# Kernel tuning notes

Measured on AMD Instinct MI355X. Metric: run time of the kernel, lower is better.

The kernel has to match this reference:

```python
import jax, jax.numpy as jnp
import numpy as np

NUM_HEADS = 8
GROUPS = 8
EPS = 1e-5


def setup_inputs() -> dict:
    key = jax.random.key(0)
    ks = jax.random.split(key, 5)
    B, C, H, W = 2, 512, 64, 64
    x = jax.random.normal(ks[0], (B, C, H, W), dtype=jnp.float32)
    gn_w = jnp.ones((C,), dtype=jnp.float32)
    gn_b = jnp.zeros((C,), dtype=jnp.float32)
    qkv_w = jax.random.normal(ks[1], (3 * C, C), dtype=jnp.float32) * 0.02  # 1x1 conv weight
    qkv_b = jnp.zeros((3 * C,), dtype=jnp.float32)
    proj_w = jax.random.normal(ks[2], (C, C), dtype=jnp.float32) * 0.02
    proj_b = jnp.zeros((C,), dtype=jnp.float32)
    return {"x": x, "gn_w": gn_w, "gn_b": gn_b, "qkv_w": qkv_w,
            "qkv_b": qkv_b, "proj_w": proj_w, "proj_b": proj_b}


def group_norm(x, w, b):
    B, C, H, W = x.shape
    xg = x.reshape(B, GROUPS, C // GROUPS, H, W)
    mean = xg.mean(axis=(2, 3, 4), keepdims=True)
    var = xg.var(axis=(2, 3, 4), keepdims=True)  # biased, matching torch GroupNorm
    h = ((xg - mean) * jax.lax.rsqrt(var + EPS)).reshape(B, C, H, W)
    return h * w[None, :, None, None] + b[None, :, None, None]


def reference(x, gn_w, gn_b, qkv_w, qkv_b, proj_w, proj_b):
    B, C, H, W = x.shape
    nh = NUM_HEADS
    dh = C // nh
    scale = dh ** -0.5
    S = H * W

    h = group_norm(x, gn_w, gn_b)
    # 1x1 conv == per-pixel linear: (B,3C,H,W)
    qkv = jnp.einsum('bchw,oc->bohw', h, qkv_w) + qkv_b[None, :, None, None]
    qkv = qkv.reshape(B, 3, nh, dh, S)
    q = jnp.swapaxes(qkv[:, 0], -1, -2)  # (B, nh, S, dh)
    k = jnp.swapaxes(qkv[:, 1], -1, -2)
    v = jnp.swapaxes(qkv[:, 2], -1, -2)

    attn = jax.nn.softmax(jnp.einsum('bhsd,btd->bhst', q, k.reshape(B * nh, S, dh).reshape(B, nh, S, dh)) * scale, axis=-1) if False else jax.nn.softmax(jnp.einsum('bhsd,bhtd->bhst', q, k) * scale, axis=-1)
    out = jnp.einsum('bhst,bhtd->bhsd', attn, v)  # (B, nh, S, dh)
    out = jnp.swapaxes(out, -1, -2).reshape(B, C, H, W)
    out = jnp.einsum('bchw,oc->bohw', out, proj_w) + proj_b[None, :, None, None]
    return x + out
```

## Files before the change

kernel.cpp:

```cpp
#include <hip/hip_runtime.h>
#include <hip/hip_bf16.h>

typedef __attribute__((ext_vector_type(4)))  float  f32x4;
typedef __attribute__((ext_vector_type(16))) float  f32x16;
typedef __attribute__((ext_vector_type(8)))  short  s16x8;
typedef __attribute__((ext_vector_type(4)))  short  s16x4;
typedef __attribute__((ext_vector_type(4)))  unsigned u32x4;
typedef __attribute__((ext_vector_type(2)))  unsigned u32x2;

__device__ __forceinline__ float bf2f(short v) {
    unsigned u = ((unsigned)(unsigned short)v) << 16;
    return __builtin_bit_cast(float, u);
}
__device__ __forceinline__ short f2bf(float f) {
    unsigned u = __builtin_bit_cast(unsigned, f);
    u += 0x7fff + ((u >> 16) & 1);
    return (short)(u >> 16);
}
__device__ __forceinline__ unsigned cvt_pk_bf16(float lo, float hi) {
    unsigned r;
    asm("v_cvt_pk_bf16_f32 %0, %1, %2" : "=v"(r) : "v"(lo), "v"(hi));
    return r;
}
__device__ __forceinline__ float exp2_asm(float x) {
    float r; asm("v_exp_f32 %0, %1" : "=v"(r) : "v"(x)); return r;
}
__device__ __forceinline__ float log2_asm(float x) {
    float r; asm("v_log_f32 %0, %1" : "=v"(r) : "v"(x)); return r;
}
__device__ __forceinline__ void perm32swap(unsigned &a, unsigned &b) {
    u32x2 r = __builtin_amdgcn_permlane32_swap(a, b, false, false);
    a = r[0]; b = r[1];
}
__device__ __forceinline__ void gload16(const short* g, short* l) {
    __builtin_amdgcn_global_load_lds(
        (const __attribute__((address_space(1))) void*)g,
        (__attribute__((address_space(3))) void*)l, 16, 0, 0);
}

#define BATCH 2
#define CCH   512
#define SSP   4096
#define NH    8
#define DH    64

__global__ __launch_bounds__(256) void gn_partial_wcast_kernel(
    const float* __restrict__ x, float* __restrict__ part,
    const float* __restrict__ qw, const float* __restrict__ pw,
    short* __restrict__ dq, short* __restrict__ dp)
{
    if (blockIdx.x >= 512) {
        int idx = ((blockIdx.x - 512) * 256 + threadIdx.x) * 8;
        const float* src; short* dst;
        if (idx < 786432) { src = qw + idx; dst = dq + idx; }
        else              { src = pw + (idx - 786432); dst = dp + (idx - 786432); }
        f32x4 a = *(const f32x4*)src;
        f32x4 b = *(const f32x4*)(src + 4);
        s16x8 o;
        o[0]=f2bf(a[0]); o[1]=f2bf(a[1]); o[2]=f2bf(a[2]); o[3]=f2bf(a[3]);
        o[4]=f2bf(b[0]); o[5]=f2bf(b[1]); o[6]=f2bf(b[2]); o[7]=f2bf(b[3]);
        *(s16x8*)dst = o;
        return;
    }
    int bg = blockIdx.x >> 5, chunk = blockIdx.x & 31;
    const float* base = x + (size_t)bg * 262144 + chunk * 8192;
    int t = threadIdx.x, lane = t & 63, wave = t >> 6;
    float s = 0.f, ss = 0.f;
    #pragma unroll
    for (int k = 0; k < 8; ++k) {
        f32x4 v = *(const f32x4*)&base[k * 1024 + t * 4];
        #pragma unroll
        for (int j = 0; j < 4; ++j) { s += v[j]; ss += v[j] * v[j]; }
    }
    #pragma unroll
    for (int mask = 1; mask < 64; mask <<= 1) {
        s  += __shfl_xor(s,  mask);
        ss += __shfl_xor(ss, mask);
    }
    __shared__ float rs[4], rss[4];
    if (lane == 0) { rs[wave] = s; rss[wave] = ss; }
    __syncthreads();
    if (t == 0) {
        part[blockIdx.x * 2]     = rs[0] + rs[1] + rs[2] + rs[3];
        part[blockIdx.x * 2 + 1] = rss[0] + rss[1] + rss[2] + rss[3];
    }
}

__global__ void gn_final_kernel(const float* __restrict__ part, float* __restrict__ stats)
{
    int t = threadIdx.x;
    if (t < 16) {
        float s = 0.f, ss = 0.f;
        for (int c = 0; c < 32; ++c) {
            s  += part[(t * 32 + c) * 2];
            ss += part[(t * 32 + c) * 2 + 1];
        }
        float mean = s * (1.f / 262144.f);
        float var  = ss * (1.f / 262144.f) - mean * mean;
        stats[t * 2]     = mean;
        stats[t * 2 + 1] = rsqrtf(var + 1e-5f);
    }
}

__global__ __launch_bounds__(256) void gn_apply_kernel(
    const float* __restrict__ x, const float* __restrict__ gw, const float* __restrict__ gb,
    const float* __restrict__ stats, short* __restrict__ hbuf)
{
    __shared__ float tile[64][65];
    int id = blockIdx.x;
    int st = id & 63, ct = (id >> 6) & 7, b = id >> 9;
    int t  = threadIdx.x;
    float mean = stats[(b * 8 + ct) * 2], rstd = stats[(b * 8 + ct) * 2 + 1];
    #pragma unroll
    for (int pass = 0; pass < 4; ++pass) {
        int cr = pass * 16 + (t >> 4);
        int c  = ct * 64 + cr;
        f32x4 v = *(const f32x4*)&x[((size_t)(b * CCH + c)) * SSP + st * 64 + (t & 15) * 4];
        float w  = gw[c] * rstd;
        float bb = gb[c] - mean * w;
        #pragma unroll
        for (int j = 0; j < 4; ++j) tile[cr][(t & 15) * 4 + j] = v[j] * w + bb;
    }
    __syncthreads();
    int sr = t >> 2, cc0 = (t & 3) * 16;
    s16x8 o0, o1;
    #pragma unroll
    for (int j = 0; j < 8; ++j) {
        o0[j] = f2bf(tile[cc0 + j][sr]);
        o1[j] = f2bf(tile[cc0 + 8 + j][sr]);
    }
    short* dst = &hbuf[(size_t)(b * SSP + st * 64 + sr) * CCH + ct * 64 + cc0];
    *(s16x8*)dst = o0;
    *(s16x8*)(dst + 8) = o1;
}

template<int EPI>
__global__ __launch_bounds__(256) void gemm_bt_kernel(
    const short* __restrict__ A, const short* __restrict__ Bt,
    const float* __restrict__ bias,
    short* __restrict__ qout, short* __restrict__ kout, short* __restrict__ vout,
    const float* __restrict__ xres, float* __restrict__ out,
    int K)
{
    __shared__ short As[4096], Bs[4096];
    const int t = threadIdx.x;
    const int lane = t & 63, wave = t >> 6;
    const int wm = wave >> 1, wn = wave & 1;
    const int flat = blockIdx.y * 64 + blockIdx.x;
    const int m0 = (((flat & 7) << 3) + ((flat >> 3) & 7)) * 128;
    const int n0 = (flat >> 6) * 128;
    const int l15 = lane & 15, lq = lane >> 4;

    f32x4 acc[4][4];
    #pragma unroll
    for (int i = 0; i < 4; ++i)
        #pragma unroll
        for (int j = 0; j < 4; ++j) acc[i][j] = (f32x4){0.f, 0.f, 0.f, 0.f};

    for (int kk = 0; kk < K; kk += 32) {
        __syncthreads();
        #pragma unroll
        for (int i = 0; i < 2; ++i) {
            int idx = i * 256 + t;
            int row = idx >> 2, cb = idx & 3;
            int dst = ((row >> 4) << 9) + ((((row & 15)) | (cb << 4)) << 3);
            *(s16x8*)&As[dst] = *(const s16x8*)&A [(size_t)(m0 + row) * K + kk + cb * 8];
            *(s16x8*)&Bs[dst] = *(const s16x8*)&Bt[(size_t)(n0 + row) * K + kk + cb * 8];
        }
        __syncthreads();
        s16x8 af[4], bfr[4];
        #pragma unroll
        for (int mt = 0; mt < 4; ++mt) af[mt]  = *(const s16x8*)&As[(((wm * 4 + mt) << 9) + lane * 8)];
        #pragma unroll
        for (int nt = 0; nt < 4; ++nt) bfr[nt] = *(const s16x8*)&Bs[(((wn * 4 + nt) << 9) + lane * 8)];
        #pragma unroll
        for (int mt = 0; mt < 4; ++mt)
            #pragma unroll
            for (int nt = 0; nt < 4; ++nt)
                acc[mt][nt] = __builtin_amdgcn_mfma_f32_16x16x32_bf16(af[mt], bfr[nt], acc[mt][nt], 0, 0, 0);
    }

    #pragma unroll
    for (int mt = 0; mt < 4; ++mt) {
        const int r0 = m0 + wm * 64 + mt * 16 + lq * 4;
        #pragma unroll
        for (int nt = 0; nt < 4; ++nt) {
            const int c = n0 + wn * 64 + nt * 16 + l15;
            float bv = bias[c];
            if (EPI == 0) {
                int bb = r0 >> 12, tloc = r0 & 4095;
                if (c < 512) {
                    #pragma unroll
                    for (int i = 0; i < 4; ++i)
                        qout[(size_t)(r0 + i) * 512 + c] = f2bf(acc[mt][nt][i] + bv);
                } else if (c < 1024) {
                    int hh = (c - 512) >> 6, d = (c - 512) & 63;
                    int T = tloc >> 6, tb = (tloc >> 5) & 1;
                    size_t base = (((size_t)(bb * 8 + hh) * 64 + T) * 8 + tb * 4 + (d >> 4)) * 512
                                  + 256 * ((d >> 3) & 1) + (d & 7);
                    #pragma unroll
                    for (int i = 0; i < 4; ++i)
                        kout[base + ((tloc & 31) + i) * 8] = f2bf(acc[mt][nt][i] + bv);
                } else {
                    int hh = (c - 1024) >> 6, d = (c - 1024) & 63;
                    int T = tloc >> 6, s = (tloc >> 4) & 3, thi = (tloc >> 3) & 1, j0 = tloc & 7;
                    size_t base = (((size_t)(bb * 8 + hh) * 64 + T) * 8 + (d >> 5) * 4 + s) * 512
                                  + ((d & 31) + 32 * thi) * 8 + j0;
                    s16x4 pv;
                    #pragma unroll
                    for (int i = 0; i < 4; ++i) pv[i] = f2bf(acc[mt][nt][i] + bv);
                    *(s16x4*)&vout[base] = pv;
                }
            } else {
                int bb = r0 >> 12, s = r0 & 4095;
                size_t xi = (size_t)(bb * CCH + c) * SSP + s;
                f32x4 xv = *(const f32x4*)&xres[xi];
                f32x4 o  = xv + acc[mt][nt] + bv;
                *(f32x4*)&out[xi] = o;
            }
        }
    }
}

__global__ __launch_bounds__(256, 4) void attn_kernel(
    const short* __restrict__ qbuf, const short* __restrict__ kfrag,
    const short* __restrict__ vfrag,
    short* __restrict__ p0, short* __restrict__ p1, float* __restrict__ aout)
{
    __shared__ short Ks[2][4096];
    __shared__ short Vs[2][4096];
    const int t = threadIdx.x, lane = t & 63, wave = t >> 6;
    const int flat = blockIdx.y * 32 + blockIdx.x;
    const int p = flat >> 3;
    const int yy = (flat & 7) * 4 + (p & 3);
    const int qblk = p >> 2;
    const int bh = yy & 15, half = yy >> 4;
    const int b = bh >> 3, h = bh & 7;
    const int q0w = qblk * 128 + wave * 32;
    const int l31 = lane & 31, lh = lane >> 5;
    const int kv0 = half * 2048;

    s16x8 qf[4];
    {
        const short* qp = qbuf + (size_t)(b * SSP + q0w + l31) * 512 + h * 64 + 8 * lh;
        #pragma unroll
        for (int s = 0; s < 4; ++s) {
            s16x8 raw = *(const s16x8*)(qp + 16 * s);
            #pragma unroll
            for (int j = 0; j < 8; ++j) qf[s][j] = f2bf(bf2f(raw[j]) * 0.18033688011112042f);
        }
    }

    const short* kbase = kfrag + (size_t)bh * 262144 + lane * 8;
    const short* vbase = vfrag + (size_t)bh * 262144 + lane * 8;

    f32x16 oacc[2];
    oacc[0] = (f32x16){}; oacc[1] = (f32x16){};
    f32x16 lacc = (f32x16){};

    s16x8 ones;
    #pragma unroll
    for (int j = 0; j < 8; ++j) ones[j] = (short)0x3F80;

    {
        const short* kg = kbase + (size_t)(kv0 >> 6) * 4096 + wave * 1024;
        gload16(kg,       &Ks[0][wave * 1024]);
        gload16(kg + 512, &Ks[0][wave * 1024 + 512]);
        const short* vg = vbase + (size_t)(kv0 >> 6) * 4096 + wave * 1024;
        gload16(vg,       &Vs[0][wave * 1024]);
        gload16(vg + 512, &Vs[0][wave * 1024 + 512]);
    }
    asm volatile("s_waitcnt vmcnt(0)" ::: "memory");
    __syncthreads();

    int cur = 0;
    for (int t0 = kv0; t0 < kv0 + 2048; t0 += 64) {
        if (t0 + 64 < kv0 + 2048) {
            int nb = cur ^ 1;
            const short* kg = kbase + (size_t)((t0 + 64) >> 6) * 4096 + wave * 1024;
            gload16(kg,       &Ks[nb][wave * 1024]);
            gload16(kg + 512, &Ks[nb][wave * 1024 + 512]);
            const short* vg = vbase + (size_t)((t0 + 64) >> 6) * 4096 + wave * 1024;
            gload16(vg,       &Vs[nb][wave * 1024]);
            gload16(vg + 512, &Vs[nb][wave * 1024 + 512]);
        }

        f32x16 sacc0 = (f32x16){}, sacc1 = (f32x16){};
        __builtin_amdgcn_s_setprio(1);
        #pragma unroll
        for (int s = 0; s < 4; ++s) {
            s16x8 k0 = *(const s16x8*)&Ks[cur][(0 + s) * 512 + lane * 8];
            s16x8 k1 = *(const s16x8*)&Ks[cur][(4 + s) * 512 + lane * 8];
            sacc0 = __builtin_amdgcn_mfma_f32_32x32x16_bf16(k0, qf[s], sacc0, 0, 0, 0);
            sacc1 = __builtin_amdgcn_mfma_f32_32x32x16_bf16(k1, qf[s], sacc1, 0, 0, 0);
        }
        __builtin_amdgcn_s_setprio(0);

        #pragma unroll
        for (int r = 0; r < 16; ++r) { sacc0[r] = exp2_asm(sacc0[r]); sacc1[r] = exp2_asm(sacc1[r]); }

        unsigned w[16];
        #pragma unroll
        for (int r = 0; r < 8; ++r) {
            w[r]     = cvt_pk_bf16(sacc0[2 * r], sacc0[2 * r + 1]);
            w[8 + r] = cvt_pk_bf16(sacc1[2 * r], sacc1[2 * r + 1]);
        }
        #pragma unroll
        for (int s = 0; s < 4; ++s) {
            perm32swap(w[s * 4 + 0], w[s * 4 + 2]);
            perm32swap(w[s * 4 + 1], w[s * 4 + 3]);
        }

        __builtin_amdgcn_s_setprio(1);
        #pragma unroll
        for (int s = 0; s < 4; ++s) {
            u32x4 pb = { w[s * 4 + 0], w[s * 4 + 1], w[s * 4 + 2], w[s * 4 + 3] };
            s16x8 pB = __builtin_bit_cast(s16x8, pb);
            s16x8 v0v = *(const s16x8*)&Vs[cur][(0 + s) * 512 + lane * 8];
            s16x8 v1v = *(const s16x8*)&Vs[cur][(4 + s) * 512 + lane * 8];
            oacc[0] = __builtin_amdgcn_mfma_f32_32x32x16_bf16(v0v, pB, oacc[0], 0, 0, 0);
            oacc[1] = __builtin_amdgcn_mfma_f32_32x32x16_bf16(v1v, pB, oacc[1], 0, 0, 0);
            lacc    = __builtin_amdgcn_mfma_f32_32x32x16_bf16(ones, pB, lacc, 0, 0, 0);
        }
        __builtin_amdgcn_s_setprio(0);

        asm volatile("s_waitcnt vmcnt(0)" ::: "memory");
        __syncthreads();
        cur ^= 1;
    }

    short* pO = half ? p1 : p0;
    float l_ = lacc[0];
    float linv = 1.f / l_;
    int q = q0w + l31;
    size_t obase = ((size_t)bh * 4096 + q) * 64;
    #pragma unroll
    for (int db = 0; db < 2; ++db)
        #pragma unroll
        for (int g = 0; g < 4; ++g) {
            s16x4 o;
            #pragma unroll
            for (int i = 0; i < 4; ++i) o[i] = f2bf(oacc[db][g * 4 + i] * linv);
            *(s16x4*)&pO[obase + db * 32 + g * 8 + lh * 4] = o;
        }
    if (lh == 0)
        aout[half * 65536 + bh * 4096 + q] = log2_asm(l_);
}

__global__ __launch_bounds__(256) void combine_kernel(
    const short* __restrict__ p0, const short* __restrict__ p1,
    const float* __restrict__ aout, short* __restrict__ ao)
{
    int bh = blockIdx.x >> 7, q = (blockIdx.x & 127) * 32 + (threadIdx.x >> 3);
    int d0 = (threadIdx.x & 7) * 8;
    size_t pi = ((size_t)bh * 4096 + q) * 64 + d0;
    s16x8 o1 = *(const s16x8*)&p0[pi];
    s16x8 o2 = *(const s16x8*)&p1[pi];
    float a1 = aout[bh * 4096 + q], a2 = aout[65536 + bh * 4096 + q];
    float M = fmaxf(a1, a2);
    float w1 = exp2_asm(a1 - M), w2 = exp2_asm(a2 - M);
    float inv = 1.f / (w1 + w2);
    w1 *= inv; w2 *= inv;
    s16x8 o;
    #pragma unroll
    for (int j = 0; j < 8; ++j) o[j] = f2bf(bf2f(o1[j]) * w1 + bf2f(o2[j]) * w2);
    int b = bh >> 3, h = bh & 7;
    *(s16x8*)&ao[(size_t)(b * SSP + q) * 512 + h * 64 + d0] = o;
}

extern "C" void kernel_launch(void* const* d_in, const int* in_sizes, int n_in,
                              void* d_out, int out_size, void* d_ws, size_t ws_size,
                              hipStream_t stream)
{
    (void)in_sizes; (void)n_in; (void)out_size; (void)ws_size;
    const float* x      = (const float*)d_in[0];
    const float* gn_w   = (const float*)d_in[1];
    const float* gn_b   = (const float*)d_in[2];
    const float* qkv_w  = (const float*)d_in[3];
    const float* qkv_b  = (const float*)d_in[4];
    const float* proj_w = (const float*)d_in[5];
    const float* proj_b = (const float*)d_in[6];
    float* out = (float*)d_out;
    char* ws = (char*)d_ws;

    short* hbuf  = (short*)(ws + 0);
    short* qbuf  = (short*)(ws + 8388608);
    short* kfrag = (short*)(ws + 16777216);
    short* vfrag = (short*)(ws + 25165824);
    short* aobuf = (short*)(ws + 33554432);
    short* wqkv  = (short*)(ws + 41943040);
    short* wproj = (short*)(ws + 43515904);
    float* part  = (float*)(ws + 44040192);
    float* stats = (float*)(ws + 44044288);
    float* ascal = (float*)(ws + 41943040);

    gn_partial_wcast_kernel<<<1024, 256, 0, stream>>>(x, part, qkv_w, proj_w, wqkv, wproj);
    gn_final_kernel<<<1, 64, 0, stream>>>(part, stats);
    gn_apply_kernel<<<1024, 256, 0, stream>>>(x, gn_w, gn_b, stats, hbuf);
    gemm_bt_kernel<0><<<dim3(64, 12), 256, 0, stream>>>(hbuf, wqkv, qkv_b,
                                                        qbuf, kfrag, vfrag, nullptr, nullptr, 512);
    attn_kernel<<<dim3(32, 32), 256, 0, stream>>>(qbuf, kfrag, vfrag,
                                                  hbuf, aobuf, ascal);
    combine_kernel<<<2048, 256, 0, stream>>>(hbuf, aobuf, ascal, kfrag);
    gemm_bt_kernel<1><<<dim3(64, 4), 256, 0, stream>>>(kfrag, wproj, proj_b,
                                                       nullptr, nullptr, nullptr, x, out, 512);
}
```

Measured before the change: 149.1 us.

## Software-pipeline attention: overlap QK of next tile with PV of previous, scalar row-sum

Restructures the attention inner loop so that the QK^T MFMAs for tile T are issued together with the PV MFMAs for tile T-1. This lets the exp2 and bf16 packing of one tile overlap with matrix work, and it needs a third V shared-memory buffer plus ping-pong P registers. The row-sum is also no longer computed by an extra MFMA against a ones vector. Instead it is accumulated with scalar adds over the exp values and combined across half-waves with a shuffle. The cost is higher register pressure from carrying the P fragments across iterations, plus more LDS use, which could reduce occupancy.

```diff
diff --git a/kernel.cpp b/kernel.cpp
--- a/kernel.cpp
+++ b/kernel.cpp
@@ -228,7 +228,7 @@
     short* __restrict__ p0, short* __restrict__ p1, float* __restrict__ aout)
 {
     __shared__ short Ks[2][4096];
-    __shared__ short Vs[2][4096];
+    __shared__ short Vs[3][4096];
     const int t = threadIdx.x, lane = t & 63, wave = t >> 6;
     const int flat = blockIdx.y * 32 + blockIdx.x;
     const int p = flat >> 3;
@@ -238,7 +238,7 @@
     const int b = bh >> 3, h = bh & 7;
     const int q0w = qblk * 128 + wave * 32;
     const int l31 = lane & 31, lh = lane >> 5;
-    const int kv0 = half * 2048;
+    const int tile0 = half * 32;
 
     s16x8 qf[4];
     {
@@ -256,81 +256,100 @@
 
     f32x16 oacc[2];
     oacc[0] = (f32x16){}; oacc[1] = (f32x16){};
-    f32x16 lacc = (f32x16){};
-
-    s16x8 ones;
-    #pragma unroll
-    for (int j = 0; j < 8; ++j) ones[j] = (short)0x3F80;
+    float l_ = 0.f;
+    s16x8 pA[4], pB[4];
+
+    int kcur = 0, knext = 1, vprev = 2, vcur = 0, vnext = 1;
 
     {
-        const short* kg = kbase + (size_t)(kv0 >> 6) * 4096 + wave * 1024;
+        const short* kg = kbase + (size_t)tile0 * 4096 + wave * 1024;
         gload16(kg,       &Ks[0][wave * 1024]);
         gload16(kg + 512, &Ks[0][wave * 1024 + 512]);
-        const short* vg = vbase + (size_t)(kv0 >> 6) * 4096 + wave * 1024;
+        const short* vg = vbase + (size_t)tile0 * 4096 + wave * 1024;
         gload16(vg,       &Vs[0][wave * 1024]);
         gload16(vg + 512, &Vs[0][wave * 1024 + 512]);
     }
     asm volatile("s_waitcnt vmcnt(0)" ::: "memory");
     __syncthreads();
 
-    int cur = 0;
-    for (int t0 = kv0; t0 < kv0 + 2048; t0 += 64) {
-        if (t0 + 64 < kv0 + 2048) {
-            int nb = cur ^ 1;
-            const short* kg = kbase + (size_t)((t0 + 64) >> 6) * 4096 + wave * 1024;
-            gload16(kg,       &Ks[nb][wave * 1024]);
-            gload16(kg + 512, &Ks[nb][wave * 1024 + 512]);
-            const short* vg = vbase + (size_t)((t0 + 64) >> 6) * 4096 + wave * 1024;
-            gload16(vg,       &Vs[nb][wave * 1024]);
-            gload16(vg + 512, &Vs[nb][wave * 1024 + 512]);
-        }
-
-        f32x16 sacc0 = (f32x16){}, sacc1 = (f32x16){};
-        __builtin_amdgcn_s_setprio(1);
-        #pragma unroll
-        for (int s = 0; s < 4; ++s) {
-            s16x8 k0 = *(const s16x8*)&Ks[cur][(0 + s) * 512 + lane * 8];
-            s16x8 k1 = *(const s16x8*)&Ks[cur][(4 + s) * 512 + lane * 8];
-            sacc0 = __builtin_amdgcn_mfma_f32_32x32x16_bf16(k0, qf[s], sacc0, 0, 0, 0);
-            sacc1 = __builtin_amdgcn_mfma_f32_32x32x16_bf16(k1, qf[s], sacc1, 0, 0, 0);
-        }
-        __builtin_amdgcn_s_setprio(0);
-
-        #pragma unroll
-        for (int r = 0; r < 16; ++r) { sacc0[r] = exp2_asm(sacc0[r]); sacc1[r] = exp2_asm(sacc1[r]); }
-
-        unsigned w[16];
-        #pragma unroll
-        for (int r = 0; r < 8; ++r) {
-            w[r]     = cvt_pk_bf16(sacc0[2 * r], sacc0[2 * r + 1]);
-            w[8 + r] = cvt_pk_bf16(sacc1[2 * r], sacc1[2 * r + 1]);
-        }
-        #pragma unroll
-        for (int s = 0; s < 4; ++s) {
-            perm32swap(w[s * 4 + 0], w[s * 4 + 2]);
-            perm32swap(w[s * 4 + 1], w[s * 4 + 3]);
-        }
-
-        __builtin_amdgcn_s_setprio(1);
-        #pragma unroll
-        for (int s = 0; s < 4; ++s) {
-            u32x4 pb = { w[s * 4 + 0], w[s * 4 + 1], w[s * 4 + 2], w[s * 4 + 3] };
-            s16x8 pB = __builtin_bit_cast(s16x8, pb);
-            s16x8 v0v = *(const s16x8*)&Vs[cur][(0 + s) * 512 + lane * 8];
-            s16x8 v1v = *(const s16x8*)&Vs[cur][(4 + s) * 512 + lane * 8];
-            oacc[0] = __builtin_amdgcn_mfma_f32_32x32x16_bf16(v0v, pB, oacc[0], 0, 0, 0);
-            oacc[1] = __builtin_amdgcn_mfma_f32_32x32x16_bf16(v1v, pB, oacc[1], 0, 0, 0);
-            lacc    = __builtin_amdgcn_mfma_f32_32x32x16_bf16(ones, pB, lacc, 0, 0, 0);
-        }
-        __builtin_amdgcn_s_setprio(0);
-
-        asm volatile("s_waitcnt vmcnt(0)" ::: "memory");
-        __syncthreads();
-        cur ^= 1;
-    }
-
+#define ATTN_STEP(T, PIN, POUT, HAS_NEXT, DO_PV)                                  \
+    {                                                                             \
+        if (HAS_NEXT) {                                                           \
+            const short* kg = kbase + (size_t)(tile0 + (T) + 1) * 4096 + wave * 1024; \
+            gload16(kg,       &Ks[knext][wave * 1024]);                           \
+            gload16(kg + 512, &Ks[knext][wave * 1024 + 512]);                     \
+            const short* vg = vbase + (size_t)(tile0 + (T) + 1) * 4096 + wave * 1024; \
+            gload16(vg,       &Vs[vnext][wave * 1024]);                           \
+            gload16(vg + 512, &Vs[vnext][wave * 1024 + 512]);                     \
+        }                                                                         \
+        f32x16 sacc0 = (f32x16){}, sacc1 = (f32x16){};                            \
+        __builtin_amdgcn_s_setprio(1);                                            \
+        _Pragma("unroll")                                                         \
+        for (int s = 0; s < 4; ++s) {                                             \
+            s16x8 k0 = *(const s16x8*)&Ks[kcur][(0 + s) * 512 + lane * 8];        \
+            s16x8 k1 = *(const s16x8*)&Ks[kcur][(4 + s) * 512 + lane * 8];        \
+            sacc0 = __builtin_amdgcn_mfma_f32_32x32x16_bf16(k0, qf[s], sacc0, 0, 0, 0); \
+            sacc1 = __builtin_amdgcn_mfma_f32_32x32x16_bf16(k1, qf[s], sacc1, 0, 0, 0); \
+        }                                                                         \
+        if (DO_PV) {                                                              \
+            _Pragma("unroll")                                                     \
+            for (int s = 0; s < 4; ++s) {                                         \
+                s16x8 v0v = *(const s16x8*)&Vs[vprev][(0 + s) * 512 + lane * 8];  \
+                s16x8 v1v = *(const s16x8*)&Vs[vprev][(4 + s) * 512 + lane * 8];  \
+                oacc[0] = __builtin_amdgcn_mfma_f32_32x32x16_bf16(v0v, PIN[s], oacc[0], 0, 0, 0); \
+                oacc[1] = __builtin_amdgcn_mfma_f32_32x32x16_bf16(v1v, PIN[s], oacc[1], 0, 0, 0); \
+            }                                                                     \
+        }                                                                         \
+        __builtin_amdgcn_s_setprio(0);                                            \
+        float a0 = 0.f, a1 = 0.f, a2 = 0.f, a3 = 0.f;                             \
+        _Pragma("unroll")                                                         \
+        for (int r = 0; r < 8; ++r) {                                             \
+            sacc0[r]     = exp2_asm(sacc0[r]);     a0 += sacc0[r];                \
+            sacc0[8 + r] = exp2_asm(sacc0[8 + r]); a1 += sacc0[8 + r];            \
+            sacc1[r]     = exp2_asm(sacc1[r]);     a2 += sacc1[r];                \
+            sacc1[8 + r] = exp2_asm(sacc1[8 + r]); a3 += sacc1[8 + r];            \
+        }                                                                         \
+        l_ += (a0 + a1) + (a2 + a3);                                              \
+        unsigned w_[16];                                                          \
+        _Pragma("unroll")                                                         \
+        for (int r = 0; r < 8; ++r) {                                             \
+            w_[r]     = cvt_pk_bf16(sacc0[2 * r], sacc0[2 * r + 1]);              \
+            w_[8 + r] = cvt_pk_bf16(sacc1[2 * r], sacc1[2 * r + 1]);              \
+        }                                                                         \
+        _Pragma("unroll")                                                         \
+        for (int s = 0; s < 4; ++s) {                                             \
+            perm32swap(w_[s * 4 + 0], w_[s * 4 + 2]);                             \
+            perm32swap(w_[s * 4 + 1], w_[s * 4 + 3]);                             \
+            u32x4 pb4 = { w_[s * 4 + 0], w_[s * 4 + 1], w_[s * 4 + 2], w_[s * 4 + 3] }; \
+            POUT[s] = __builtin_bit_cast(s16x8, pb4);                             \
+        }                                                                         \
+        asm volatile("s_waitcnt vmcnt(0)" ::: "memory");                          \
+        __syncthreads();                                                          \
+        kcur ^= 1; knext ^= 1;                                                    \
+        int vtmp = vprev; vprev = vcur; vcur = vnext; vnext = vtmp;               \
+    }
+
+    ATTN_STEP(0, pA, pA, true, false)
+    for (int tp = 0; tp < 15; ++tp) {
+        int t1 = 2 * tp + 1;
+        ATTN_STEP(t1,     pA, pB, true, true)
+        ATTN_STEP(t1 + 1, pB, pA, true, true)
+    }
+    ATTN_STEP(31, pA, pB, false, true)
+#undef ATTN_STEP
+
+    __builtin_amdgcn_s_setprio(1);
+    #pragma unroll
+    for (int s = 0; s < 4; ++s) {
+        s16x8 v0v = *(const s16x8*)&Vs[vprev][(0 + s) * 512 + lane * 8];
+        s16x8 v1v = *(const s16x8*)&Vs[vprev][(4 + s) * 512 + lane * 8];
+        oacc[0] = __builtin_amdgcn_mfma_f32_32x32x16_bf16(v0v, pB[s], oacc[0], 0, 0, 0);
+        oacc[1] = __builtin_amdgcn_mfma_f32_32x32x16_bf16(v1v, pB[s], oacc[1], 0, 0, 0);
+    }
+    __builtin_amdgcn_s_setprio(0);
+
+    l_ += __shfl_xor(l_, 32);
     short* pO = half ? p1 : p0;
-    float l_ = lacc[0];
     float linv = 1.f / l_;
     int q = q0w + l31;
     size_t obase = ((size_t)bh * 4096 + q) * 64;
```

Result: no change. 146.4 us (-1.9%).

## Double query rows per wave in attention, fuse GN finalize into apply

Applied to the files above, without the earlier changes.

Each attention wave now handles 64 query rows instead of 32, so every K/V tile loaded into LDS feeds twice as many MFMAs and the grid is halved. The row-sum is accumulated with VALU adds instead of an extra MFMA against a ones vector, saving one matrix op per step. The separate GroupNorm finalize launch is removed; each apply block reduces the 32 partials itself with shuffles, and the apply kernel packs bf16 pairs before the LDS transpose to shrink the tile. Register pressure rises and occupancy drops to 2 blocks per CU, so latency hiding may suffer.

```diff
diff --git a/kernel.cpp b/kernel.cpp
--- a/kernel.cpp
+++ b/kernel.cpp
@@ -86,52 +86,55 @@
     }
 }
 
-__global__ void gn_final_kernel(const float* __restrict__ part, float* __restrict__ stats)
-{
-    int t = threadIdx.x;
-    if (t < 16) {
-        float s = 0.f, ss = 0.f;
-        for (int c = 0; c < 32; ++c) {
-            s  += part[(t * 32 + c) * 2];
-            ss += part[(t * 32 + c) * 2 + 1];
-        }
-        float mean = s * (1.f / 262144.f);
-        float var  = ss * (1.f / 262144.f) - mean * mean;
-        stats[t * 2]     = mean;
-        stats[t * 2 + 1] = rsqrtf(var + 1e-5f);
-    }
-}
-
 __global__ __launch_bounds__(256) void gn_apply_kernel(
     const float* __restrict__ x, const float* __restrict__ gw, const float* __restrict__ gb,
-    const float* __restrict__ stats, short* __restrict__ hbuf)
-{
-    __shared__ float tile[64][65];
+    const float* __restrict__ part, short* __restrict__ hbuf)
+{
+    __shared__ unsigned tile[32][66];
     int id = blockIdx.x;
     int st = id & 63, ct = (id >> 6) & 7, b = id >> 9;
     int t  = threadIdx.x;
-    float mean = stats[(b * 8 + ct) * 2], rstd = stats[(b * 8 + ct) * 2 + 1];
-    #pragma unroll
-    for (int pass = 0; pass < 4; ++pass) {
-        int cr = pass * 16 + (t >> 4);
-        int c  = ct * 64 + cr;
-        f32x4 v = *(const f32x4*)&x[((size_t)(b * CCH + c)) * SSP + st * 64 + (t & 15) * 4];
-        float w  = gw[c] * rstd;
-        float bb = gb[c] - mean * w;
-        #pragma unroll
-        for (int j = 0; j < 4; ++j) tile[cr][(t & 15) * 4 + j] = v[j] * w + bb;
+
+    int bg = b * 8 + ct;
+    float s  = part[(bg * 32 + (t & 31)) * 2];
+    float ss = part[(bg * 32 + (t & 31)) * 2 + 1];
+    #pragma unroll
+    for (int m = 1; m < 32; m <<= 1) { s += __shfl_xor(s, m); ss += __shfl_xor(ss, m); }
+    float mean = s * (1.f / 262144.f);
+    float var  = ss * (1.f / 262144.f) - mean * mean;
+    float rstd = rsqrtf(var + 1e-5f);
+
+    #pragma unroll
+    for (int pass = 0; pass < 2; ++pass) {
+        int cp = pass * 16 + (t >> 4);
+        int c  = ct * 64 + cp * 2;
+        const float* xp = &x[((size_t)(b * CCH + c)) * SSP + st * 64 + (t & 15) * 4];
+        f32x4 v0 = *(const f32x4*)xp;
+        f32x4 v1 = *(const f32x4*)(xp + SSP);
+        float w0 = gw[c] * rstd,     bb0 = gb[c] - mean * w0;
+        float w1 = gw[c + 1] * rstd, bb1 = gb[c + 1] - mean * w1;
+        int sp0 = (t & 15) * 4;
+        unsigned p0 = cvt_pk_bf16(v0[0] * w0 + bb0, v1[0] * w1 + bb1);
+        unsigned p1 = cvt_pk_bf16(v0[1] * w0 + bb0, v1[1] * w1 + bb1);
+        unsigned p2 = cvt_pk_bf16(v0[2] * w0 + bb0, v1[2] * w1 + bb1);
+        unsigned p3 = cvt_pk_bf16(v0[3] * w0 + bb0, v1[3] * w1 + bb1);
+        *(u32x2*)&tile[cp][sp0]     = (u32x2){p0, p1};
+        *(u32x2*)&tile[cp][sp0 + 2] = (u32x2){p2, p3};
     }
     __syncthreads();
-    int sr = t >> 2, cc0 = (t & 3) * 16;
-    s16x8 o0, o1;
-    #pragma unroll
-    for (int j = 0; j < 8; ++j) {
-        o0[j] = f2bf(tile[cc0 + j][sr]);
-        o1[j] = f2bf(tile[cc0 + 8 + j][sr]);
-    }
-    short* dst = &hbuf[(size_t)(b * SSP + st * 64 + sr) * CCH + ct * 64 + cc0];
-    *(s16x8*)dst = o0;
-    *(s16x8*)(dst + 8) = o1;
+
+    int sr = t >> 2, c16 = (t & 3) * 8;
+    unsigned r0 = tile[c16 + 0][sr];
+    unsigned r1 = tile[c16 + 1][sr];
+    unsigned r2 = tile[c16 + 2][sr];
+    unsigned r3 = tile[c16 + 3][sr];
+    unsigned r4 = tile[c16 + 4][sr];
+    unsigned r5 = tile[c16 + 5][sr];
+    unsigned r6 = tile[c16 + 6][sr];
+    unsigned r7 = tile[c16 + 7][sr];
+    short* dst = &hbuf[(size_t)(b * SSP + st * 64 + sr) * CCH + ct * 64 + c16 * 2];
+    *(u32x4*)dst       = (u32x4){r0, r1, r2, r3};
+    *(u32x4*)(dst + 8) = (u32x4){r4, r5, r6, r7};
 }
 
 template<int EPI>
@@ -222,7 +225,7 @@
     }
 }
 
-__global__ __launch_bounds__(256, 4) void attn_kernel(
+__global__ __launch_bounds__(256, 2) void attn_kernel(
     const short* __restrict__ qbuf, const short* __restrict__ kfrag,
     const short* __restrict__ vfrag,
     short* __restrict__ p0, short* __restrict__ p1, float* __restrict__ aout)
@@ -230,43 +233,43 @@
     __shared__ short Ks[2][4096];
     __shared__ short Vs[2][4096];
     const int t = threadIdx.x, lane = t & 63, wave = t >> 6;
-    const int flat = blockIdx.y * 32 + blockIdx.x;
+    const int flat = blockIdx.y * 16 + blockIdx.x;
     const int p = flat >> 3;
     const int yy = (flat & 7) * 4 + (p & 3);
     const int qblk = p >> 2;
     const int bh = yy & 15, half = yy >> 4;
     const int b = bh >> 3, h = bh & 7;
-    const int q0w = qblk * 128 + wave * 32;
+    const int q0w = qblk * 256 + wave * 64;
     const int l31 = lane & 31, lh = lane >> 5;
-    const int kv0 = half * 2048;
-
-    s16x8 qf[4];
+    const int tile0 = half * 32;
+
+    s16x8 qfa[4], qfb[4];
     {
-        const short* qp = qbuf + (size_t)(b * SSP + q0w + l31) * 512 + h * 64 + 8 * lh;
+        const short* qpa = qbuf + (size_t)(b * SSP + q0w + l31) * 512 + h * 64 + 8 * lh;
+        const short* qpb = qpa + 32 * 512;
         #pragma unroll
         for (int s = 0; s < 4; ++s) {
-            s16x8 raw = *(const s16x8*)(qp + 16 * s);
+            s16x8 ra = *(const s16x8*)(qpa + 16 * s);
+            s16x8 rb = *(const s16x8*)(qpb + 16 * s);
             #pragma unroll
-            for (int j = 0; j < 8; ++j) qf[s][j] = f2bf(bf2f(raw[j]) * 0.18033688011112042f);
+            for (int j = 0; j < 8; ++j) {
+                qfa[s][j] = f2bf(bf2f(ra[j]) * 0.18033688011112042f);
+                qfb[s][j] = f2bf(bf2f(rb[j]) * 0.18033688011112042f);
+            }
         }
     }
 
     const short* kbase = kfrag + (size_t)bh * 262144 + lane * 8;
     const short* vbase = vfrag + (size_t)bh * 262144 + lane * 8;
 
-    f32x16 oacc[2];
-    oacc[0] = (f32x16){}; oacc[1] = (f32x16){};
-    f32x16 lacc = (f32x16){};
-
-    s16x8 ones;
-    #pragma unroll
-    for (int j = 0; j < 8; ++j) ones[j] = (short)0x3F80;
+    f32x16 oa0 = (f32x16){}, oa1 = (f32x16){}, ob0 = (f32x16){}, ob1 = (f32x16){};
+    float la = 0.f, lb = 0.f;
 
     {
-        const short* kg = kbase + (size_t)(kv0 >> 6) * 4096 + wave * 1024;
+        const short* kg = kbase + (size_t)tile0 * 4096 + wave * 1024;
         gload16(kg,       &Ks[0][wave * 1024]);
         gload16(kg + 512, &Ks[0][wave * 1024 + 512]);
-        const short* vg = vbase + (size_t)(kv0 >> 6) * 4096 + wave * 1024;
+        const short* vg = vbase + (size_t)tile0 * 4096 + wave * 1024;
         gload16(vg,       &Vs[0][wave * 1024]);
         gload16(vg + 512, &Vs[0][wave * 1024 + 512]);
     }
@@ -274,53 +277,71 @@
     __syncthreads();
 
     int cur = 0;
-    for (int t0 = kv0; t0 < kv0 + 2048; t0 += 64) {
-        if (t0 + 64 < kv0 + 2048) {
+    for (int ti = 0; ti < 32; ++ti) {
+        if (ti + 1 < 32) {
             int nb = cur ^ 1;
-            const short* kg = kbase + (size_t)((t0 + 64) >> 6) * 4096 + wave * 1024;
+            const short* kg = kbase + (size_t)(tile0 + ti + 1) * 4096 + wave * 1024;
             gload16(kg,       &Ks[nb][wave * 1024]);
             gload16(kg + 512, &Ks[nb][wave * 1024 + 512]);
-            const short* vg = vbase + (size_t)((t0 + 64) >> 6) * 4096 + wave * 1024;
+            const short* vg = vbase + (size_t)(tile0 + ti + 1) * 4096 + wave * 1024;
             gload16(vg,       &Vs[nb][wave * 1024]);
             gload16(vg + 512, &Vs[nb][wave * 1024 + 512]);
         }
 
-        f32x16 sacc0 = (f32x16){}, sacc1 = (f32x16){};
+        f32x16 sa0 = (f32x16){}, sa1 = (f32x16){}, sb0 = (f32x16){}, sb1 = (f32x16){};
         __builtin_amdgcn_s_setprio(1);
         #pragma unroll
         for (int s = 0; s < 4; ++s) {
             s16x8 k0 = *(const s16x8*)&Ks[cur][(0 + s) * 512 + lane * 8];
             s16x8 k1 = *(const s16x8*)&Ks[cur][(4 + s) * 512 + lane * 8];
-            sacc0 = __builtin_amdgcn_mfma_f32_32x32x16_bf16(k0, qf[s], sacc0, 0, 0, 0);
-            sacc1 = __builtin_amdgcn_mfma_f32_32x32x16_bf16(k1, qf[s], sacc1, 0, 0, 0);
+            sa0 = __builtin_amdgcn_mfma_f32_32x32x16_bf16(k0, qfa[s], sa0, 0, 0, 0);
+            sa1 = __builtin_amdgcn_mfma_f32_32x32x16_bf16(k1, qfa[s], sa1, 0, 0, 0);
+            sb0 = __builtin_amdgcn_mfma_f32_32x32x16_bf16(k0, qfb[s], sb0, 0, 0, 0);
+            sb1 = __builtin_amdgcn_mfma_f32_32x32x16_bf16(k1, qfb[s], sb1, 0, 0, 0);
         }
         __builtin_amdgcn_s_setprio(0);
 
-        #pragma unroll
-        for (int r = 0; r < 16; ++r) { sacc0[r] = exp2_asm(sacc0[r]); sacc1[r] = exp2_asm(sacc1[r]); }
-
-        unsigned w[16];
+        float aa0 = 0.f, aa1 = 0.f, ab0 = 0.f, ab1 = 0.f;
+        #pragma unroll
+        for (int r = 0; r < 16; ++r) {
+            sa0[r] = exp2_asm(sa0[r]); aa0 += sa0[r];
+            sa1[r] = exp2_asm(sa1[r]); aa1 += sa1[r];
+            sb0[r] = exp2_asm(sb0[r]); ab0 += sb0[r];
+            sb1[r] = exp2_asm(sb1[r]); ab1 += sb1[r];
+        }
+        la += aa0 + aa1;
+        lb += ab0 + ab1;
+
+        unsigned wa[16], wb[16];
         #pragma unroll
         for (int r = 0; r < 8; ++r) {
-            w[r]     = cvt_pk_bf16(sacc0[2 * r], sacc0[2 * r + 1]);
-            w[8 + r] = cvt_pk_bf16(sacc1[2 * r], sacc1[2 * r + 1]);
-        }
+            wa[r]     = cvt_pk_bf16(sa0[2 * r], sa0[2 * r + 1]);
+            wa[8 + r] = cvt_pk_bf16(sa1[2 * r], sa1[2 * r + 1]);
+            wb[r]     = cvt_pk_bf16(sb0[2 * r], sb0[2 * r + 1]);
+            wb[8 + r] = cvt_pk_bf16(sb1[2 * r], sb1[2 * r + 1]);
+        }
+        s16x8 pa[4], pb[4];
         #pragma unroll
         for (int s = 0; s < 4; ++s) {
-            perm32swap(w[s * 4 + 0], w[s * 4 + 2]);
-            perm32swap(w[s * 4 + 1], w[s * 4 + 3]);
+            perm32swap(wa[s * 4 + 0], wa[s * 4 + 2]);
+            perm32swap(wa[s * 4 + 1], wa[s * 4 + 3]);
+            u32x4 pa4 = { wa[s * 4 + 0], wa[s * 4 + 1], wa[s * 4 + 2], wa[s * 4 + 3] };
+            pa[s] = __builtin_bit_cast(s16x8, pa4);
+            perm32swap(wb[s * 4 + 0], wb[s * 4 + 2]);
+            perm32swap(wb[s * 4 + 1], wb[s * 4 + 3]);
+            u32x4 pb4 = { wb[s * 4 + 0], wb[s * 4 + 1], wb[s * 4 + 2], wb[s * 4 + 3] };
+            pb[s] = __builtin_bit_cast(s16x8, pb4);
         }
 
         __builtin_amdgcn_s_setprio(1);
         #pragma unroll
         for (int s = 0; s < 4; ++s) {
-            u32x4 pb = { w[s * 4 + 0], w[s * 4 + 1], w[s * 4 + 2], w[s * 4 + 3] };
-            s16x8 pB = __builtin_bit_cast(s16x8, pb);
             s16x8 v0v = *(const s16x8*)&Vs[cur][(0 + s) * 512 + lane * 8];
             s16x8 v1v = *(const s16x8*)&Vs[cur][(4 + s) * 512 + lane * 8];
-            oacc[0] = __builtin_amdgcn_mfma_f32_32x32x16_bf16(v0v, pB, oacc[0], 0, 0, 0);
-            oacc[1] = __builtin_amdgcn_mfma_f32_32x32x16_bf16(v1v, pB, oacc[1], 0, 0, 0);
-            lacc    = __builtin_amdgcn_mfma_f32_32x32x16_bf16(ones, pB, lacc, 0, 0, 0);
+            oa0 = __builtin_amdgcn_mfma_f32_32x32x16_bf16(v0v, pa[s], oa0, 0, 0, 0);
+            oa1 = __builtin_amdgcn_mfma_f32_32x32x16_bf16(v1v, pa[s], oa1, 0, 0, 0);
+            ob0 = __builtin_amdgcn_mfma_f32_32x32x16_bf16(v0v, pb[s], ob0, 0, 0, 0);
+            ob1 = __builtin_amdgcn_mfma_f32_32x32x16_bf16(v1v, pb[s], ob1, 0, 0, 0);
         }
         __builtin_amdgcn_s_setprio(0);
 
@@ -330,21 +351,44 @@
     }
 
     short* pO = half ? p1 : p0;
-    float l_ = lacc[0];
-    float linv = 1.f / l_;
-    int q = q0w + l31;
-    size_t obase = ((size_t)bh * 4096 + q) * 64;
-    #pragma unroll
-    for (int db = 0; db < 2; ++db)
+    {
+        la += __shfl_xor(la, 32);
+        float linv = 1.f / la;
+        int q = q0w + l31;
+        size_t obase = ((size_t)bh * 4096 + q) * 64;
         #pragma unroll
         for (int g = 0; g < 4; ++g) {
-            s16x4 o;
+            s16x4 o0v, o1v;
             #pragma unroll
-            for (int i = 0; i < 4; ++i) o[i] = f2bf(oacc[db][g * 4 + i] * linv);
-            *(s16x4*)&pO[obase + db * 32 + g * 8 + lh * 4] = o;
-        }
-    if (lh == 0)
-        aout[half * 65536 + bh * 4096 + q] = log2_asm(l_);
+            for (int i = 0; i < 4; ++i) {
+                o0v[i] = f2bf(oa0[g * 4 + i] * linv);
+                o1v[i] = f2bf(oa1[g * 4 + i] * linv);
+            }
+            *(s16x4*)&pO[obase + g * 8 + lh * 4]      = o0v;
+            *(s16x4*)&pO[obase + 32 + g * 8 + lh * 4] = o1v;
+        }
+        if (lh == 0)
+            aout[half * 65536 + bh * 4096 + q] = log2_asm(la);
+    }
+    {
+        lb += __shfl_xor(lb, 32);
+        float linv = 1.f / lb;
+        int q = q0w + 32 + l31;
+        size_t obase = ((size_t)bh * 4096 + q) * 64;
+        #pragma unroll
+        for (int g = 0; g < 4; ++g) {
+            s16x4 o0v, o1v;
+            #pragma unroll
+            for (int i = 0; i < 4; ++i) {
+                o0v[i] = f2bf(ob0[g * 4 + i] * linv);
+                o1v[i] = f2bf(ob1[g * 4 + i] * linv);
+            }
+            *(s16x4*)&pO[obase + g * 8 + lh * 4]      = o0v;
+            *(s16x4*)&pO[obase + 32 + g * 8 + lh * 4] = o1v;
+        }
+        if (lh == 0)
+            aout[half * 65536 + bh * 4096 + q] = log2_asm(lb);
+    }
 }
 
 __global__ __launch_bounds__(256) void combine_kernel(
@@ -391,15 +435,13 @@
     short* wqkv  = (short*)(ws + 41943040);
     short* wproj = (short*)(ws + 43515904);
     float* part  = (float*)(ws + 44040192);
-    float* stats = (float*)(ws + 44044288);
     float* ascal = (float*)(ws + 41943040);
 
     gn_partial_wcast_kernel<<<1024, 256, 0, stream>>>(x, part, qkv_w, proj_w, wqkv, wproj);
-    gn_final_kernel<<<1, 64, 0, stream>>>(part, stats);
-    gn_apply_kernel<<<1024, 256, 0, stream>>>(x, gn_w, gn_b, stats, hbuf);
+    gn_apply_kernel<<<1024, 256, 0, stream>>>(x, gn_w, gn_b, part, hbuf);
     gemm_bt_kernel<0><<<dim3(64, 12), 256, 0, stream>>>(hbuf, wqkv, qkv_b,
                                                         qbuf, kfrag, vfrag, nullptr, nullptr, 512);
-    attn_kernel<<<dim3(32, 32), 256, 0, stream>>>(qbuf, kfrag, vfrag,
+    attn_kernel<<<dim3(16, 32), 256, 0, stream>>>(qbuf, kfrag, vfrag,
                                                   hbuf, aobuf, ascal);
     combine_kernel<<<2048, 256, 0, stream>>>(hbuf, aobuf, ascal, kfrag);
     gemm_bt_kernel<1><<<dim3(64, 4), 256, 0, stream>>>(kfrag, wproj, proj_b,
```

Measured after the change: 140.0 us (median of 2 runs). -6.1%, faster.
